# Optimization experiments

Hardware: AMD Instinct MI355X
Metric: run time of the kernel (lower is better)

The kernel has to match this reference:

```python
import jax, jax.numpy as jnp
import numpy as np
import math

H, SQK, SV, PQK, PV = 12, 16, 16, 4, 8
C1, C2 = 384, 128
B, N = 1, 768


def _rand_rot(key, shape):
    # random proper rotation matrices via QR of gaussian matrices
    m = jax.random.normal(key, shape + (3, 3), dtype=jnp.float32)
    q, r = jnp.linalg.qr(m)
    d = jnp.sign(jnp.diagonal(r, axis1=-2, axis2=-1))
    return q * d[..., None, :]


def setup_inputs() -> dict:
    key = jax.random.key(0)
    ks = jax.random.split(key, 16)
    s = 0.05
    return {
        'act': jax.random.normal(ks[0], (B, N, C1), dtype=jnp.float32),
        'act_2d': jax.random.normal(ks[1], (B, N, N, C2), dtype=jnp.float32),
        'sequence_mask': jnp.ones((B, N, 1), dtype=jnp.float32),
        'rot': _rand_rot(ks[2], (B, N)),
        'trans': jax.random.normal(ks[3], (B, N, 3), dtype=jnp.float32),
        'wq': jax.random.normal(ks[4], (C1, H * SQK), dtype=jnp.float32) * s,
        'wk': jax.random.normal(ks[5], (C1, H * SQK), dtype=jnp.float32) * s,
        'wv': jax.random.normal(ks[6], (C1, H * SV), dtype=jnp.float32) * s,
        'wqp': jax.random.normal(ks[7], (C1, H * PQK * 3), dtype=jnp.float32) * s,
        'bqp': jnp.zeros((H * PQK * 3,), dtype=jnp.float32),
        'wkp': jax.random.normal(ks[8], (C1, H * PQK * 3), dtype=jnp.float32) * s,
        'bkp': jnp.zeros((H * PQK * 3,), dtype=jnp.float32),
        'wvp': jax.random.normal(ks[9], (C1, H * PV * 3), dtype=jnp.float32) * s,
        'bvp': jnp.zeros((H * PV * 3,), dtype=jnp.float32),
        'w2d': jax.random.normal(ks[10], (C2, H), dtype=jnp.float32) * s,
        'b2d': jnp.zeros((H,), dtype=jnp.float32),
        'wfin': jax.random.normal(ks[11], (H * (C2 + SV + 4 * PV), C1), dtype=jnp.float32) * s,
        'bfin': jnp.zeros((C1,), dtype=jnp.float32),
        'tw': jnp.zeros((H,), dtype=jnp.float32),
    }


def _points(act, w, b, P):
    # torch: view [...,H,P*3] -> split into 3 chunks of P -> stack last => layout [H,3,P]
    p = (act @ w + b).reshape(*act.shape[:-1], H, 3, P)
    p = jnp.moveaxis(p, -2, -1)  # [B,N,H,P,3]
    return p.reshape(*act.shape[:-1], H * P, 3)


def _ipa(act, act_2d, sequence_mask, rot, trans,
         wq, wk, wv, wqp, bqp, wkp, bkp, wvp, bvp, w2d, b2d, wfin, bfin, tw):
    b, n, _ = act.shape
    q = (act @ wq).reshape(b, n, H, SQK) * math.sqrt(1.0 / SQK)
    k = (act @ wk).reshape(b, n, H, SQK)
    v = (act @ wv).reshape(b, n, H, SV)

    apply = lambda p: jnp.einsum('bnij,bnpj->bnpi', rot, p) + trans[:, :, None, :]
    qp = apply(_points(act, wqp, bqp, PQK))  # [B,N,H*PQK,3]
    kp = apply(_points(act, wkp, bkp, PQK))
    vp = apply(_points(act, wvp, bvp, PV))   # [B,N,H*PV,3]

    # point-distance logits
    pw = math.sqrt(2.0 / (9.0 * PQK)) * jax.nn.softplus(tw)  # [H]
    d2 = jnp.sum(jnp.square(qp[:, :, None] - kp[:, None]), -1)  # [B,N,N,H*PQK]
    d2 = d2.reshape(b, n, n, H, PQK).sum(-1)                    # [B,N,N,H]
    logits = -0.5 * pw * d2
    logits = logits + jnp.einsum('bqhc,bkhc->bqkh', q, k)
    logits = logits + act_2d @ w2d + b2d
    mask_2d = sequence_mask * jnp.swapaxes(sequence_mask, -1, -2)  # [B,N,N]
    logits = logits - 1e5 * (1.0 - mask_2d)[..., None]
    logits = logits * math.sqrt(1.0 / 3.0)
    attn = jax.nn.softmax(logits, axis=-2)  # over key residues

    res_scalar = jnp.einsum('bqkh,bkhc->bqhc', attn, v).reshape(b, n, H * SV)
    vp5 = vp.reshape(b, n, H, PV, 3)
    rpg = jnp.einsum('bqkh,bkhpd->bqhpd', attn, vp5).reshape(b, n, H * PV, 3)
    rpl = jnp.einsum('bnji,bnpj->bnpi', rot, rpg - trans[:, :, None, :])  # invert_apply
    norms = jnp.linalg.norm(rpl, axis=-1)
    r2d = jnp.einsum('bijh,bijc->bihc', attn, act_2d).reshape(b, n, H * C2)
    final = jnp.concatenate(
        [res_scalar, rpl[..., 0], rpl[..., 1], rpl[..., 2], norms, r2d], axis=-1)
    return final @ wfin + bfin


def reference(act, act_2d, sequence_mask, rot, trans,
              wq, wk, wv, wqp, bqp, wkp, bkp, wvp, bvp, w2d, b2d, wfin, bfin, tw):
    return _ipa(act, act_2d, sequence_mask, rot, trans,
                wq, wk, wv, wqp, bqp, wkp, bkp, wvp, bvp, w2d, b2d, wfin, bfin, tw)
```

## Files before the change

### kernel.cpp

```cpp
#include <hip/hip_runtime.h>
#include <math.h>

#define NH    12
#define NRES  768
#define C1V   384
#define C2V   128
#define NPROJ 1152
#define QKD   28
#define FDIM  2112
#define VVD   480
#define APAD  772
#define KSPLIT 11

typedef __attribute__((ext_vector_type(8))) short bf16x8;
typedef __attribute__((ext_vector_type(4))) float f32x4;

__device__ __forceinline__ float softplusf_(float x) {
    return (x > 20.f) ? x : log1pf(__expf(x));
}
__device__ __forceinline__ ushort f2bf(float x) {
    union { float f; unsigned u; } v; v.f = x;
    unsigned r = (v.u + 0x7fffu + ((v.u >> 16) & 1u)) >> 16;
    return (ushort)r;
}

__global__ __launch_bounds__(256) void k1_proj(
    const float* __restrict__ act,
    const float* __restrict__ wq, const float* __restrict__ wk,
    const float* __restrict__ wv, const float* __restrict__ wqp,
    const float* __restrict__ wkp, const float* __restrict__ wvp,
    const float* __restrict__ bqp, const float* __restrict__ bkp,
    const float* __restrict__ bvp, const float* __restrict__ w2d,
    float* __restrict__ proj, ushort* __restrict__ w2dT)
{
    __shared__ float As[64 * 33];
    __shared__ float Bs[32 * 68];
    const int n0 = blockIdx.x * 64, m0 = blockIdx.y * 64;
    const int tid = threadIdx.x;
    const int tx = tid & 15, ty = tid >> 4;
    float c[4][4] = {};

    for (int kt = 0; kt < C1V; kt += 32) {
        for (int idx = tid; idx < 64 * 32; idx += 256) {
            int r = idx >> 5, j = idx & 31;
            As[r * 33 + j] = act[(m0 + r) * C1V + kt + j];
        }
        for (int idx = tid; idx < 32 * 64; idx += 256) {
            int r = idx >> 6, col = idx & 63;
            int jj = n0 + col, k = kt + r;
            float w;
            if      (jj < 192) w = wq [k * 192 + jj];
            else if (jj < 384) w = wk [k * 192 + jj - 192];
            else if (jj < 576) w = wv [k * 192 + jj - 384];
            else if (jj < 720) w = wqp[k * 144 + jj - 576];
            else if (jj < 864) w = wkp[k * 144 + jj - 720];
            else               w = wvp[k * 288 + jj - 864];
            Bs[r * 68 + col] = w;
        }
        __syncthreads();
        #pragma unroll
        for (int kk = 0; kk < 32; ++kk) {
            float a[4];
            #pragma unroll
            for (int i = 0; i < 4; ++i) a[i] = As[(ty * 4 + i) * 33 + kk];
            float4 b4 = *(const float4*)&Bs[kk * 68 + tx * 4];
            float b[4] = {b4.x, b4.y, b4.z, b4.w};
            #pragma unroll
            for (int i = 0; i < 4; ++i)
                #pragma unroll
                for (int j = 0; j < 4; ++j) c[i][j] += a[i] * b[j];
        }
        __syncthreads();
    }
    float biasv[4];
    #pragma unroll
    for (int j = 0; j < 4; ++j) {
        int col = n0 + tx * 4 + j;
        biasv[j] = (col >= 864) ? bvp[col - 864]
                 : (col >= 720) ? bkp[col - 720]
                 : (col >= 576) ? bqp[col - 576] : 0.f;
    }
    #pragma unroll
    for (int i = 0; i < 4; ++i) {
        float4 v;
        v.x = c[i][0] + biasv[0]; v.y = c[i][1] + biasv[1];
        v.z = c[i][2] + biasv[2]; v.w = c[i][3] + biasv[3];
        *(float4*)&proj[(m0 + ty * 4 + i) * NPROJ + n0 + tx * 4] = v;
    }
    if (n0 == 0 && m0 == 0) {
        for (int idx = tid; idx < 2048; idx += 256) {
            int h = idx >> 7, cc = idx & 127;
            w2dT[idx] = (h < NH) ? f2bf(w2d[cc * NH + h]) : (ushort)0;
        }
    }
}

__global__ __launch_bounds__(64) void k2_prep(
    const float* __restrict__ proj, const float* __restrict__ rot,
    const float* __restrict__ trans, const float* __restrict__ tw,
    float* __restrict__ Qv, float* __restrict__ Kv,
    float* __restrict__ akArr, float* __restrict__ vv)
{
    const int n = blockIdx.x, tid = threadIdx.x;
    __shared__ float kp2[48];
    const float* pr = proj + n * NPROJ;
    float R[9], T[3];
    #pragma unroll
    for (int i = 0; i < 9; ++i) R[i] = rot[n * 9 + i];
    #pragma unroll
    for (int i = 0; i < 3; ++i) T[i] = trans[n * 3 + i];

    for (int idx = tid; idx < 192; idx += 64) {
        int h = idx >> 4, cc = idx & 15;
        Qv[(n * NH + h) * QKD + cc] = pr[idx] * 0.25f;
        Kv[(n * NH + h) * QKD + cc] = pr[192 + idx];
        vv[n * VVD + idx] = pr[384 + idx];
    }
    if (tid < 48) {
        int h = tid >> 2, p = tid & 3;
        float pwh = 0.23570226039551584f * softplusf_(tw[h]);
        float lx = pr[576 + h * 12 + p];
        float ly = pr[576 + h * 12 + 4 + p];
        float lz = pr[576 + h * 12 + 8 + p];
        float gx = R[0] * lx + R[1] * ly + R[2] * lz + T[0];
        float gy = R[3] * lx + R[4] * ly + R[5] * lz + T[1];
        float gz = R[6] * lx + R[7] * ly + R[8] * lz + T[2];
        float* qd = &Qv[(n * NH + h) * QKD + 16];
        qd[p] = pwh * gx; qd[4 + p] = pwh * gy; qd[8 + p] = pwh * gz;
        lx = pr[720 + h * 12 + p];
        ly = pr[720 + h * 12 + 4 + p];
        lz = pr[720 + h * 12 + 8 + p];
        gx = R[0] * lx + R[1] * ly + R[2] * lz + T[0];
        gy = R[3] * lx + R[4] * ly + R[5] * lz + T[1];
        gz = R[6] * lx + R[7] * ly + R[8] * lz + T[2];
        float* kd = &Kv[(n * NH + h) * QKD + 16];
        kd[p] = gx; kd[4 + p] = gy; kd[8 + p] = gz;
        kp2[tid] = gx * gx + gy * gy + gz * gz;
    }
    __syncthreads();
    if (tid < NH) {
        float pwh = 0.23570226039551584f * softplusf_(tw[tid]);
        akArr[n * NH + tid] = -0.5f * pwh *
            (kp2[tid * 4] + kp2[tid * 4 + 1] + kp2[tid * 4 + 2] + kp2[tid * 4 + 3]);
    }
    for (int idx = tid; idx < 96; idx += 64) {
        int h = idx >> 3, p = idx & 7;
        float lx = pr[864 + h * 24 + p];
        float ly = pr[864 + h * 24 + 8 + p];
        float lz = pr[864 + h * 24 + 16 + p];
        float gx = R[0] * lx + R[1] * ly + R[2] * lz + T[0];
        float gy = R[3] * lx + R[4] * ly + R[5] * lz + T[1];
        float gz = R[6] * lx + R[7] * ly + R[8] * lz + T[2];
        float* dst = &vv[n * VVD + 192 + h * 24 + p * 3];
        dst[0] = gx; dst[1] = gy; dst[2] = gz;
    }
}

__global__ __launch_bounds__(256) void k2b_qk(
    const float* __restrict__ Qv, const float* __restrict__ Kv,
    const float* __restrict__ akArr, float* __restrict__ qkBuf)
{
    const int h = blockIdx.z;
    const int k0 = blockIdx.x * 64, q0 = blockIdx.y * 64;
    __shared__ float As[64 * 29];
    __shared__ float Bs[64 * 29];
    const int tid = threadIdx.x, tx = tid & 15, ty = tid >> 4;

    for (int idx = tid; idx < 64 * 28; idx += 256) {
        int r = idx / 28, j = idx - r * 28;
        As[r * 29 + j] = Qv[((q0 + r) * NH + h) * QKD + j];
        Bs[r * 29 + j] = Kv[((k0 + r) * NH + h) * QKD + j];
    }
    __syncthreads();
    float c[4][4] = {};
    #pragma unroll
    for (int kk = 0; kk < 28; ++kk) {
        float a[4], b[4];
        #pragma unroll
        for (int i = 0; i < 4; ++i) a[i] = As[(ty * 4 + i) * 29 + kk];
        #pragma unroll
        for (int j = 0; j < 4; ++j) b[j] = Bs[(tx * 4 + j) * 29 + kk];
        #pragma unroll
        for (int i = 0; i < 4; ++i)
            #pragma unroll
            for (int j = 0; j < 4; ++j) c[i][j] += a[i] * b[j];
    }
    float akv[4];
    #pragma unroll
    for (int j = 0; j < 4; ++j) akv[j] = akArr[(k0 + tx * 4 + j) * NH + h];
    #pragma unroll
    for (int i = 0; i < 4; ++i) {
        float4 v;
        v.x = c[i][0] + akv[0]; v.y = c[i][1] + akv[1];
        v.z = c[i][2] + akv[2]; v.w = c[i][3] + akv[3];
        *(float4*)&qkBuf[((q0 + ty * 4 + i) * NH + h) * NRES + k0 + tx * 4] = v;
    }
}

__global__ __launch_bounds__(256) void kA_mfma(
    const float* __restrict__ act2d, const float* __restrict__ smask,
    const ushort* __restrict__ w2dT, float* __restrict__ qkBuf)
{
    const int q = blockIdx.y, k0 = blockIdx.x * 64, tid = threadIdx.x;
    __shared__ ushort tile[64 * 136];
    const int lane = tid & 63, wv = tid >> 6;
    const int nb = lane & 15, quad = lane >> 4;

    bf16x8 bfr[4];
    #pragma unroll
    for (int s = 0; s < 4; ++s)
        bfr[s] = *(const bf16x8*)&w2dT[nb * 128 + quad * 8 + s * 32];

    const float* src = act2d + ((size_t)q * NRES + k0) * C2V;
    #pragma unroll
    for (int i = 0; i < 8; ++i) {
        int f = tid + i * 256;
        int r = f >> 5, c4 = f & 31;
        float4 v = ((const float4*)src)[f];
        ushort4 o = { f2bf(v.x), f2bf(v.y), f2bf(v.z), f2bf(v.w) };
        *(ushort4*)&tile[r * 136 + c4 * 4] = o;
    }
    __syncthreads();

    f32x4 acc = {0.f, 0.f, 0.f, 0.f};
    #pragma unroll
    for (int s = 0; s < 4; ++s) {
        bf16x8 af = *(const bf16x8*)&tile[(wv * 16 + nb) * 136 + quad * 8 + s * 32];
        acc = __builtin_amdgcn_mfma_f32_16x16x32_bf16(af, bfr[s], acc, 0, 0, 0);
    }

    if (nb < NH) {
        const int kb = k0 + wv * 16 + quad * 4;
        float* dst = &qkBuf[((size_t)(q * NH + nb)) * NRES + kb];
        float4 old = *(float4*)dst;
        float4 sm = *(const float4*)&smask[kb];
        const float smq = smask[q];
        const float scale = 0.5773502691896258f;
        float4 outv;
        outv.x = (old.x + acc[0] - 1e5f * (1.f - smq * sm.x)) * scale;
        outv.y = (old.y + acc[1] - 1e5f * (1.f - smq * sm.y)) * scale;
        outv.z = (old.z + acc[2] - 1e5f * (1.f - smq * sm.z)) * scale;
        outv.w = (old.w + acc[3] - 1e5f * (1.f - smq * sm.w)) * scale;
        *(float4*)dst = outv;
    }
}

__global__ __launch_bounds__(256) void kC_attn(
    const float* __restrict__ act2d, const float* __restrict__ qkBuf,
    const float* __restrict__ vv, const float* __restrict__ rot,
    const float* __restrict__ trans, float* __restrict__ F)
{
    const int q = blockIdx.x, tid = threadIdx.x;
    __shared__ float attnS[NH * APAD];
    __shared__ float scr[1536];
    __shared__ float red[NH * 4];
    __shared__ float mh[NH], lh[NH];
    __shared__ float rotS[9], transS[3];

    if (tid < 9) rotS[tid] = rot[q * 9 + tid];
    if (tid < 3) transS[tid] = trans[q * 3 + tid];

    float lg[3][NH];
    #pragma unroll
    for (int h = 0; h < NH; ++h)
        #pragma unroll
        for (int i = 0; i < 3; ++i)
            lg[i][h] = qkBuf[((size_t)(q * NH + h)) * NRES + tid + 256 * i];

    const int wv_ = tid >> 6, lane = tid & 63;
    #pragma unroll
    for (int h = 0; h < NH; ++h) {
        float v = fmaxf(fmaxf(lg[0][h], lg[1][h]), lg[2][h]);
        for (int off = 32; off > 0; off >>= 1) v = fmaxf(v, __shfl_down(v, off, 64));
        if (lane == 0) red[h * 4 + wv_] = v;
    }
    __syncthreads();
    if (tid < NH)
        mh[tid] = fmaxf(fmaxf(red[tid * 4], red[tid * 4 + 1]),
                        fmaxf(red[tid * 4 + 2], red[tid * 4 + 3]));
    __syncthreads();
    float lsum[NH];
    #pragma unroll
    for (int h = 0; h < NH; ++h) lsum[h] = 0.f;
    #pragma unroll
    for (int i = 0; i < 3; ++i)
        #pragma unroll
        for (int h = 0; h < NH; ++h) {
            float e = __expf(lg[i][h] - mh[h]);
            attnS[h * APAD + tid + 256 * i] = e;
            lsum[h] += e;
        }
    #pragma unroll
    for (int h = 0; h < NH; ++h) {
        float v = lsum[h];
        for (int off = 32; off > 0; off >>= 1) v += __shfl_down(v, off, 64);
        if (lane == 0) red[h * 4 + wv_] = v;
    }
    __syncthreads();
    if (tid < NH)
        lh[tid] = 1.f / (red[tid * 4] + red[tid * 4 + 1] + red[tid * 4 + 2] + red[tid * 4 + 3]);
    __syncthreads();

    const int cq = tid & 31, hg = (tid >> 5) & 3, kg = tid >> 7;
    const int h0 = 3 * hg;
    const float* abase = act2d + ((size_t)q * NRES + kg * 384) * C2V + cq * 4;
    const float* at0 = &attnS[(h0    ) * APAD + kg * 384];
    const float* at1 = &attnS[(h0 + 1) * APAD + kg * 384];
    const float* at2 = &attnS[(h0 + 2) * APAD + kg * 384];
    float4 a0 = {0,0,0,0}, a1 = {0,0,0,0}, a2 = {0,0,0,0};

    for (int kk = 0; kk < 384; kk += 4) {
        float4 t0 = *(const float4*)&abase[(size_t)(kk    ) * C2V];
        float4 t1 = *(const float4*)&abase[(size_t)(kk + 1) * C2V];
        float4 t2 = *(const float4*)&abase[(size_t)(kk + 2) * C2V];
        float4 t3 = *(const float4*)&abase[(size_t)(kk + 3) * C2V];
        float4 p0 = *(const float4*)&at0[kk];
        float4 p1 = *(const float4*)&at1[kk];
        float4 p2 = *(const float4*)&at2[kk];
        a0.x += p0.x*t0.x + p0.y*t1.x + p0.z*t2.x + p0.w*t3.x;
        a0.y += p0.x*t0.y + p0.y*t1.y + p0.z*t2.y + p0.w*t3.y;
        a0.z += p0.x*t0.z + p0.y*t1.z + p0.z*t2.z + p0.w*t3.z;
        a0.w += p0.x*t0.w + p0.y*t1.w + p0.z*t2.w + p0.w*t3.w;
        a1.x += p1.x*t0.x + p1.y*t1.x + p1.z*t2.x + p1.w*t3.x;
        a1.y += p1.x*t0.y + p1.y*t1.y + p1.z*t2.y + p1.w*t3.y;
        a1.z += p1.x*t0.z + p1.y*t1.z + p1.z*t2.z + p1.w*t3.z;
        a1.w += p1.x*t0.w + p1.y*t1.w + p1.z*t2.w + p1.w*t3.w;
        a2.x += p2.x*t0.x + p2.y*t1.x + p2.z*t2.x + p2.w*t3.x;
        a2.y += p2.x*t0.y + p2.y*t1.y + p2.z*t2.y + p2.w*t3.y;
        a2.z += p2.x*t0.z + p2.y*t1.z + p2.z*t2.z + p2.w*t3.z;
        a2.w += p2.x*t0.w + p2.y*t1.w + p2.z*t2.w + p2.w*t3.w;
    }
    if (kg == 1) {
        *(float4*)&scr[(h0    ) * 128 + cq * 4] = a0;
        *(float4*)&scr[(h0 + 1) * 128 + cq * 4] = a1;
        *(float4*)&scr[(h0 + 2) * 128 + cq * 4] = a2;
    }
    __syncthreads();
    float* Fq = F + q * FDIM;
    if (kg == 0) {
        float4 b0 = *(const float4*)&scr[(h0    ) * 128 + cq * 4];
        float4 b1 = *(const float4*)&scr[(h0 + 1) * 128 + cq * 4];
        float4 b2 = *(const float4*)&scr[(h0 + 2) * 128 + cq * 4];
        float l0 = lh[h0], l1 = lh[h0 + 1], l2 = lh[h0 + 2];
        float4 o0 = {(a0.x+b0.x)*l0, (a0.y+b0.y)*l0, (a0.z+b0.z)*l0, (a0.w+b0.w)*l0};
        float4 o1 = {(a1.x+b1.x)*l1, (a1.y+b1.y)*l1, (a1.z+b1.z)*l1, (a1.w+b1.w)*l1};
        float4 o2 = {(a2.x+b2.x)*l2, (a2.y+b2.y)*l2, (a2.z+b2.z)*l2, (a2.w+b2.w)*l2};
        *(float4*)&Fq[576 + (h0    ) * 128 + cq * 4] = o0;
        *(float4*)&Fq[576 + (h0 + 1) * 128 + cq * 4] = o1;
        *(float4*)&Fq[576 + (h0 + 2) * 128 + cq * 4] = o2;
    }
    __syncthreads();

    const int j4 = tid & 127;
    const int kgv = tid >> 7;
    float p0 = 0.f, p1 = 0.f, p2 = 0.f, p3 = 0.f;
    if (j4 < 120) {
        const int h = (j4 < 48) ? (j4 >> 2) : ((j4 - 48) / 6);
        const float* at = &attnS[h * APAD + kgv * 384];
        const float* col = vv + (size_t)(kgv * 384) * VVD + j4 * 4;
        #pragma unroll 8
        for (int k = 0; k < 384; ++k) {
            float a = at[k];
            float4 v = *(const float4*)(col + (size_t)k * VVD);
            p0 += a * v.x; p1 += a * v.y; p2 += a * v.z; p3 += a * v.w;
        }
    }
    __syncthreads();
    if (j4 < 120) {
        float4 pv = {p0, p1, p2, p3};
        *(float4*)&scr[(kgv * 120 + j4) * 4] = pv;
    }
    __syncthreads();
    if (tid < 120) {
        float4 a = *(const float4*)&scr[tid * 4];
        float4 b = *(const float4*)&scr[(120 + tid) * 4];
        const int h = (tid < 48) ? (tid >> 2) : ((tid - 48) / 6);
        const float il = lh[h];
        float4 s = {(a.x + b.x) * il, (a.y + b.y) * il,
                    (a.z + b.z) * il, (a.w + b.w) * il};
        if (tid < 48) {
            *(float4*)&Fq[tid * 4] = s;
        } else {
            *(float4*)&scr[1024 + (tid - 48) * 4] = s;
        }
    }
    __syncthreads();
    if (tid < 96) {
        float gx = scr[1024 + tid * 3]     - transS[0];
        float gy = scr[1024 + tid * 3 + 1] - transS[1];
        float gz = scr[1024 + tid * 3 + 2] - transS[2];
        float x = rotS[0] * gx + rotS[3] * gy + rotS[6] * gz;
        float y = rotS[1] * gx + rotS[4] * gy + rotS[7] * gz;
        float z = rotS[2] * gx + rotS[5] * gy + rotS[8] * gz;
        Fq[192 + tid] = x;
        Fq[288 + tid] = y;
        Fq[384 + tid] = z;
        Fq[480 + tid] = sqrtf(x * x + y * y + z * z);
    }
}

__global__ __launch_bounds__(256) void k5_partial(
    const float* __restrict__ F, const float* __restrict__ wfin,
    float* __restrict__ part)
{
    const int n0 = blockIdx.x * 64, m0 = blockIdx.y * 64, kz = blockIdx.z;
    const int kbeg = kz * 192;
    __shared__ float As[64 * 33];
    __shared__ float Bs[32 * 68];
    const int tid = threadIdx.x, tx = tid & 15, ty = tid >> 4;
    float c[4][4] = {};

    for (int kt = kbeg; kt < kbeg + 192; kt += 32) {
        for (int idx = tid; idx < 64 * 32; idx += 256) {
            int r = idx >> 5, j = idx & 31;
            As[r * 33 + j] = F[(m0 + r) * FDIM + kt + j];
        }
        for (int idx = tid; idx < 32 * 64; idx += 256) {
            int r = idx >> 6, col = idx & 63;
            Bs[r * 68 + col] = wfin[(kt + r) * 384 + n0 + col];
        }
        __syncthreads();
        #pragma unroll
        for (int kk = 0; kk < 32; ++kk) {
            float a[4];
            #pragma unroll
            for (int i = 0; i < 4; ++i) a[i] = As[(ty * 4 + i) * 33 + kk];
            float4 b4 = *(const float4*)&Bs[kk * 68 + tx * 4];
            float b[4] = {b4.x, b4.y, b4.z, b4.w};
            #pragma unroll
            for (int i = 0; i < 4; ++i)
                #pragma unroll
                for (int j = 0; j < 4; ++j) c[i][j] += a[i] * b[j];
        }
        __syncthreads();
    }
    float* dst = part + (size_t)kz * (768 * 384);
    #pragma unroll
    for (int i = 0; i < 4; ++i) {
        float4 v = {c[i][0], c[i][1], c[i][2], c[i][3]};
        *(float4*)&dst[(m0 + ty * 4 + i) * 384 + n0 + tx * 4] = v;
    }
}

__global__ __launch_bounds__(256) void k5_reduce(
    const float* __restrict__ part, const float* __restrict__ bfin,
    float* __restrict__ out)
{
    const int e = blockIdx.x * 256 + threadIdx.x;
    const float4* p = (const float4*)part;
    float4 b = ((const float4*)bfin)[e % 96];
    float4 s = {b.x, b.y, b.z, b.w};
    #pragma unroll
    for (int kz = 0; kz < KSPLIT; ++kz) {
        float4 v = p[(size_t)kz * 73728 + e];
        s.x += v.x; s.y += v.y; s.z += v.z; s.w += v.w;
    }
    ((float4*)out)[e] = s;
}

extern "C" void kernel_launch(void* const* d_in, const int* in_sizes, int n_in,
                              void* d_out, int out_size, void* d_ws, size_t ws_size,
                              hipStream_t stream) {
    const float* act   = (const float*)d_in[0];
    const float* act2d = (const float*)d_in[1];
    const float* smask = (const float*)d_in[2];
    const float* rot   = (const float*)d_in[3];
    const float* trans = (const float*)d_in[4];
    const float* wq    = (const float*)d_in[5];
    const float* wk    = (const float*)d_in[6];
    const float* wvv   = (const float*)d_in[7];
    const float* wqp   = (const float*)d_in[8];
    const float* bqp   = (const float*)d_in[9];
    const float* wkp   = (const float*)d_in[10];
    const float* bkp   = (const float*)d_in[11];
    const float* wvp   = (const float*)d_in[12];
    const float* bvp   = (const float*)d_in[13];
    const float* w2d   = (const float*)d_in[14];
    const float* wfin  = (const float*)d_in[16];
    const float* bfin  = (const float*)d_in[17];
    const float* tw    = (const float*)d_in[18];

    float* W     = (float*)d_ws;
    float* proj  = W;
    float* Qv    = proj  + 768 * NPROJ;
    float* Kv    = Qv    + 768 * NH * QKD;
    float* akArr = Kv    + 768 * NH * QKD;
    float* vvA   = akArr + 768 * NH;
    float* qkBuf = vvA   + 768 * VVD;
    float* F     = qkBuf + 768 * NH * NRES;
    ushort* w2dT = (ushort*)(F + 768 * FDIM);
    float* part  = qkBuf;

    k1_proj<<<dim3(18, 12), 256, 0, stream>>>(act, wq, wk, wvv, wqp, wkp, wvp,
                                              bqp, bkp, bvp, w2d, proj, w2dT);
    k2_prep<<<dim3(NRES), 64, 0, stream>>>(proj, rot, trans, tw, Qv, Kv, akArr, vvA);
    k2b_qk<<<dim3(12, 12, NH), 256, 0, stream>>>(Qv, Kv, akArr, qkBuf);
    kA_mfma<<<dim3(12, NRES), 256, 0, stream>>>(act2d, smask, w2dT, qkBuf);
    kC_attn<<<dim3(NRES), 256, 0, stream>>>(act2d, qkBuf, vvA, rot, trans, F);
    k5_partial<<<dim3(6, 12, KSPLIT), 256, 0, stream>>>(F, wfin, part);
    k5_reduce<<<dim3(288), 256, 0, stream>>>(part, bfin, (float*)d_out);
}
```

Measured before the change: 689.2 us.

## Fuse QK logits into pair-bias kernel and split-K reduce into GEMM

Removes the separate QK tiled-GEMM kernel. kA_mfma now computes each q·k dot product plus the point-attention bias inline, so qkBuf is written once instead of written, read and rewritten. The split-K final projection reduction moves into k5_partial: a per-tile atomic counter (cleared in kC_attn) lets the last arriving block sum the partials and add the bias. This drops two launches and a large intermediate round trip, at the cost of redundant K loads per block and atomics/threadfences.

Measured after the change: 872.6 us. 26.6% more time.

```diff
diff --git a/kernel.cpp b/kernel.cpp
--- a/kernel.cpp
+++ b/kernel.cpp
@@ -156,55 +156,17 @@
     }
 }
 
-__global__ __launch_bounds__(256) void k2b_qk(
-    const float* __restrict__ Qv, const float* __restrict__ Kv,
-    const float* __restrict__ akArr, float* __restrict__ qkBuf)
-{
-    const int h = blockIdx.z;
-    const int k0 = blockIdx.x * 64, q0 = blockIdx.y * 64;
-    __shared__ float As[64 * 29];
-    __shared__ float Bs[64 * 29];
-    const int tid = threadIdx.x, tx = tid & 15, ty = tid >> 4;
-
-    for (int idx = tid; idx < 64 * 28; idx += 256) {
-        int r = idx / 28, j = idx - r * 28;
-        As[r * 29 + j] = Qv[((q0 + r) * NH + h) * QKD + j];
-        Bs[r * 29 + j] = Kv[((k0 + r) * NH + h) * QKD + j];
-    }
-    __syncthreads();
-    float c[4][4] = {};
-    #pragma unroll
-    for (int kk = 0; kk < 28; ++kk) {
-        float a[4], b[4];
-        #pragma unroll
-        for (int i = 0; i < 4; ++i) a[i] = As[(ty * 4 + i) * 29 + kk];
-        #pragma unroll
-        for (int j = 0; j < 4; ++j) b[j] = Bs[(tx * 4 + j) * 29 + kk];
-        #pragma unroll
-        for (int i = 0; i < 4; ++i)
-            #pragma unroll
-            for (int j = 0; j < 4; ++j) c[i][j] += a[i] * b[j];
-    }
-    float akv[4];
-    #pragma unroll
-    for (int j = 0; j < 4; ++j) akv[j] = akArr[(k0 + tx * 4 + j) * NH + h];
-    #pragma unroll
-    for (int i = 0; i < 4; ++i) {
-        float4 v;
-        v.x = c[i][0] + akv[0]; v.y = c[i][1] + akv[1];
-        v.z = c[i][2] + akv[2]; v.w = c[i][3] + akv[3];
-        *(float4*)&qkBuf[((q0 + ty * 4 + i) * NH + h) * NRES + k0 + tx * 4] = v;
-    }
-}
-
 __global__ __launch_bounds__(256) void kA_mfma(
     const float* __restrict__ act2d, const float* __restrict__ smask,
-    const ushort* __restrict__ w2dT, float* __restrict__ qkBuf)
+    const ushort* __restrict__ w2dT, const float* __restrict__ Qv,
+    const float* __restrict__ Kv, const float* __restrict__ akArr,
+    float* __restrict__ qkBuf)
 {
     const int q = blockIdx.y, k0 = blockIdx.x * 64, tid = threadIdx.x;
     __shared__ ushort tile[64 * 136];
     const int lane = tid & 63, wv = tid >> 6;
     const int nb = lane & 15, quad = lane >> 4;
+    const int kb = k0 + wv * 16 + quad * 4;
 
     bf16x8 bfr[4];
     #pragma unroll
@@ -220,6 +182,28 @@
         ushort4 o = { f2bf(v.x), f2bf(v.y), f2bf(v.z), f2bf(v.w) };
         *(ushort4*)&tile[r * 136 + c4 * 4] = o;
     }
+
+    float qk[4] = {0.f, 0.f, 0.f, 0.f};
+    float ak[4] = {0.f, 0.f, 0.f, 0.f};
+    if (nb < NH) {
+        const float* Qr = &Qv[((size_t)q * NH + nb) * QKD];
+        float4 qv[7];
+        #pragma unroll
+        for (int j = 0; j < 7; ++j) qv[j] = *(const float4*)&Qr[j * 4];
+        #pragma unroll
+        for (int r = 0; r < 4; ++r) {
+            const float* Kr = &Kv[((size_t)(kb + r) * NH + nb) * QKD];
+            float s = 0.f;
+            #pragma unroll
+            for (int j = 0; j < 7; ++j) {
+                float4 kv = *(const float4*)&Kr[j * 4];
+                s += qv[j].x * kv.x + qv[j].y * kv.y
+                   + qv[j].z * kv.z + qv[j].w * kv.w;
+            }
+            qk[r] = s;
+            ak[r] = akArr[(size_t)(kb + r) * NH + nb];
+        }
+    }
     __syncthreads();
 
     f32x4 acc = {0.f, 0.f, 0.f, 0.f};
@@ -230,25 +214,23 @@
     }
 
     if (nb < NH) {
-        const int kb = k0 + wv * 16 + quad * 4;
-        float* dst = &qkBuf[((size_t)(q * NH + nb)) * NRES + kb];
-        float4 old = *(float4*)dst;
         float4 sm = *(const float4*)&smask[kb];
         const float smq = smask[q];
         const float scale = 0.5773502691896258f;
         float4 outv;
-        outv.x = (old.x + acc[0] - 1e5f * (1.f - smq * sm.x)) * scale;
-        outv.y = (old.y + acc[1] - 1e5f * (1.f - smq * sm.y)) * scale;
-        outv.z = (old.z + acc[2] - 1e5f * (1.f - smq * sm.z)) * scale;
-        outv.w = (old.w + acc[3] - 1e5f * (1.f - smq * sm.w)) * scale;
-        *(float4*)dst = outv;
+        outv.x = (qk[0] + ak[0] + acc[0] - 1e5f * (1.f - smq * sm.x)) * scale;
+        outv.y = (qk[1] + ak[1] + acc[1] - 1e5f * (1.f - smq * sm.y)) * scale;
+        outv.z = (qk[2] + ak[2] + acc[2] - 1e5f * (1.f - smq * sm.z)) * scale;
+        outv.w = (qk[3] + ak[3] + acc[3] - 1e5f * (1.f - smq * sm.w)) * scale;
+        *(float4*)&qkBuf[((size_t)(q * NH + nb)) * NRES + kb] = outv;
     }
 }
 
 __global__ __launch_bounds__(256) void kC_attn(
     const float* __restrict__ act2d, const float* __restrict__ qkBuf,
     const float* __restrict__ vv, const float* __restrict__ rot,
-    const float* __restrict__ trans, float* __restrict__ F)
+    const float* __restrict__ trans, float* __restrict__ F,
+    unsigned* __restrict__ cnt)
 {
     const int q = blockIdx.x, tid = threadIdx.x;
     __shared__ float attnS[NH * APAD];
@@ -257,6 +239,7 @@
     __shared__ float mh[NH], lh[NH];
     __shared__ float rotS[9], transS[3];
 
+    if (q == 0 && tid < 72) cnt[tid] = 0u;
     if (tid < 9) rotS[tid] = rot[q * 9 + tid];
     if (tid < 3) transS[tid] = trans[q * 3 + tid];
 
@@ -401,7 +384,8 @@
 
 __global__ __launch_bounds__(256) void k5_partial(
     const float* __restrict__ F, const float* __restrict__ wfin,
-    float* __restrict__ part)
+    const float* __restrict__ bfin, float* __restrict__ part,
+    unsigned* __restrict__ cnt, float* __restrict__ out)
 {
     const int n0 = blockIdx.x * 64, m0 = blockIdx.y * 64, kz = blockIdx.z;
     const int kbeg = kz * 192;
@@ -440,22 +424,29 @@
         float4 v = {c[i][0], c[i][1], c[i][2], c[i][3]};
         *(float4*)&dst[(m0 + ty * 4 + i) * 384 + n0 + tx * 4] = v;
     }
-}
-
-__global__ __launch_bounds__(256) void k5_reduce(
-    const float* __restrict__ part, const float* __restrict__ bfin,
-    float* __restrict__ out)
-{
-    const int e = blockIdx.x * 256 + threadIdx.x;
-    const float4* p = (const float4*)part;
-    float4 b = ((const float4*)bfin)[e % 96];
-    float4 s = {b.x, b.y, b.z, b.w};
-    #pragma unroll
-    for (int kz = 0; kz < KSPLIT; ++kz) {
-        float4 v = p[(size_t)kz * 73728 + e];
-        s.x += v.x; s.y += v.y; s.z += v.z; s.w += v.w;
-    }
-    ((float4*)out)[e] = s;
+
+    __threadfence();
+    __shared__ int isLast;
+    if (tid == 0) {
+        unsigned old = atomicAdd(&cnt[blockIdx.y * 6 + blockIdx.x], 1u);
+        isLast = (old == KSPLIT - 1) ? 1 : 0;
+    }
+    __syncthreads();
+    if (isLast) {
+        __threadfence();
+        #pragma unroll
+        for (int i = 0; i < 4; ++i) {
+            const int row = m0 + ty * 4 + i, colb = n0 + tx * 4;
+            float4 s = *(const float4*)&bfin[colb];
+            #pragma unroll
+            for (int kzz = 0; kzz < KSPLIT; ++kzz) {
+                float4 v = *(const float4*)&part[(size_t)kzz * (768 * 384)
+                                                 + (size_t)row * 384 + colb];
+                s.x += v.x; s.y += v.y; s.z += v.z; s.w += v.w;
+            }
+            *(float4*)&out[(size_t)row * 384 + colb] = s;
+        }
+    }
 }
 
 extern "C" void kernel_launch(void* const* d_in, const int* in_sizes, int n_in,
@@ -489,14 +480,15 @@
     float* qkBuf = vvA   + 768 * VVD;
     float* F     = qkBuf + 768 * NH * NRES;
     ushort* w2dT = (ushort*)(F + 768 * FDIM);
+    unsigned* cnt = (unsigned*)(w2dT + 2048);
     float* part  = qkBuf;
 
     k1_proj<<<dim3(18, 12), 256, 0, stream>>>(act, wq, wk, wvv, wqp, wkp, wvp,
                                               bqp, bkp, bvp, w2d, proj, w2dT);
     k2_prep<<<dim3(NRES), 64, 0, stream>>>(proj, rot, trans, tw, Qv, Kv, akArr, vvA);
-    k2b_qk<<<dim3(12, 12, NH), 256, 0, stream>>>(Qv, Kv, akArr, qkBuf);
-    kA_mfma<<<dim3(12, NRES), 256, 0, stream>>>(act2d, smask, w2dT, qkBuf);
-    kC_attn<<<dim3(NRES), 256, 0, stream>>>(act2d, qkBuf, vvA, rot, trans, F);
-    k5_partial<<<dim3(6, 12, KSPLIT), 256, 0, stream>>>(F, wfin, part);
-    k5_reduce<<<dim3(288), 256, 0, stream>>>(part, bfin, (float*)d_out);
-}
+    kA_mfma<<<dim3(12, NRES), 256, 0, stream>>>(act2d, smask, w2dT, Qv, Kv, akArr,
+                                                qkBuf);
+    kC_attn<<<dim3(NRES), 256, 0, stream>>>(act2d, qkBuf, vvA, rot, trans, F, cnt);
+    k5_partial<<<dim3(6, 12, KSPLIT), 256, 0, stream>>>(F, wfin, bfin, part, cnt,
+                                                        (float*)d_out);
+}
```

## Load act_2d straight into MFMA registers and fuse split-K reduce via atomic counters

Applied to the files above, without the earlier changes.

In kA_mfma, each lane now reads its own act_2d row slice directly from global memory and converts it to bf16 in registers. This drops the shared-memory tile and the __syncthreads. Separately, the k5_reduce kernel is removed: the last k5_partial block for each output tile, chosen with an atomic counter and thread fences, sums the split-K partials and adds the bias. The counters are zeroed inside kC_attn. This saves one kernel launch, but the per-lane global loads in kA may coalesce less well.

New measurement: 782.1 us. 13.5% more time.

```diff
diff --git a/kernel.cpp b/kernel.cpp
--- a/kernel.cpp
+++ b/kernel.cpp
@@ -202,7 +202,6 @@
     const ushort* __restrict__ w2dT, float* __restrict__ qkBuf)
 {
     const int q = blockIdx.y, k0 = blockIdx.x * 64, tid = threadIdx.x;
-    __shared__ ushort tile[64 * 136];
     const int lane = tid & 63, wv = tid >> 6;
     const int nb = lane & 15, quad = lane >> 4;
 
@@ -211,21 +210,22 @@
     for (int s = 0; s < 4; ++s)
         bfr[s] = *(const bf16x8*)&w2dT[nb * 128 + quad * 8 + s * 32];
 
-    const float* src = act2d + ((size_t)q * NRES + k0) * C2V;
-    #pragma unroll
-    for (int i = 0; i < 8; ++i) {
-        int f = tid + i * 256;
-        int r = f >> 5, c4 = f & 31;
-        float4 v = ((const float4*)src)[f];
-        ushort4 o = { f2bf(v.x), f2bf(v.y), f2bf(v.z), f2bf(v.w) };
-        *(ushort4*)&tile[r * 136 + c4 * 4] = o;
-    }
-    __syncthreads();
-
+    const int krow = k0 + wv * 16 + nb;
+    const float* arow = act2d + ((size_t)q * NRES + krow) * C2V + quad * 8;
+    float4 u[4], w[4];
+    #pragma unroll
+    for (int s = 0; s < 4; ++s) {
+        u[s] = *(const float4*)&arow[s * 32];
+        w[s] = *(const float4*)&arow[s * 32 + 4];
+    }
     f32x4 acc = {0.f, 0.f, 0.f, 0.f};
     #pragma unroll
     for (int s = 0; s < 4; ++s) {
-        bf16x8 af = *(const bf16x8*)&tile[(wv * 16 + nb) * 136 + quad * 8 + s * 32];
+        bf16x8 af;
+        af[0] = (short)f2bf(u[s].x); af[1] = (short)f2bf(u[s].y);
+        af[2] = (short)f2bf(u[s].z); af[3] = (short)f2bf(u[s].w);
+        af[4] = (short)f2bf(w[s].x); af[5] = (short)f2bf(w[s].y);
+        af[6] = (short)f2bf(w[s].z); af[7] = (short)f2bf(w[s].w);
         acc = __builtin_amdgcn_mfma_f32_16x16x32_bf16(af, bfr[s], acc, 0, 0, 0);
     }
 
@@ -248,7 +248,8 @@
 __global__ __launch_bounds__(256) void kC_attn(
     const float* __restrict__ act2d, const float* __restrict__ qkBuf,
     const float* __restrict__ vv, const float* __restrict__ rot,
-    const float* __restrict__ trans, float* __restrict__ F)
+    const float* __restrict__ trans, float* __restrict__ F,
+    unsigned* __restrict__ cnt)
 {
     const int q = blockIdx.x, tid = threadIdx.x;
     __shared__ float attnS[NH * APAD];
@@ -257,6 +258,7 @@
     __shared__ float mh[NH], lh[NH];
     __shared__ float rotS[9], transS[3];
 
+    if (q == 0 && tid < 72) cnt[tid] = 0u;
     if (tid < 9) rotS[tid] = rot[q * 9 + tid];
     if (tid < 3) transS[tid] = trans[q * 3 + tid];
 
@@ -401,7 +403,8 @@
 
 __global__ __launch_bounds__(256) void k5_partial(
     const float* __restrict__ F, const float* __restrict__ wfin,
-    float* __restrict__ part)
+    const float* __restrict__ bfin, float* __restrict__ part,
+    unsigned* __restrict__ cnt, float* __restrict__ out)
 {
     const int n0 = blockIdx.x * 64, m0 = blockIdx.y * 64, kz = blockIdx.z;
     const int kbeg = kz * 192;
@@ -440,22 +443,29 @@
         float4 v = {c[i][0], c[i][1], c[i][2], c[i][3]};
         *(float4*)&dst[(m0 + ty * 4 + i) * 384 + n0 + tx * 4] = v;
     }
-}
-
-__global__ __launch_bounds__(256) void k5_reduce(
-    const float* __restrict__ part, const float* __restrict__ bfin,
-    float* __restrict__ out)
-{
-    const int e = blockIdx.x * 256 + threadIdx.x;
-    const float4* p = (const float4*)part;
-    float4 b = ((const float4*)bfin)[e % 96];
-    float4 s = {b.x, b.y, b.z, b.w};
-    #pragma unroll
-    for (int kz = 0; kz < KSPLIT; ++kz) {
-        float4 v = p[(size_t)kz * 73728 + e];
-        s.x += v.x; s.y += v.y; s.z += v.z; s.w += v.w;
-    }
-    ((float4*)out)[e] = s;
+
+    __threadfence();
+    __shared__ int isLast;
+    if (tid == 0) {
+        unsigned old = atomicAdd(&cnt[blockIdx.y * 6 + blockIdx.x], 1u);
+        isLast = (old == KSPLIT - 1) ? 1 : 0;
+    }
+    __syncthreads();
+    if (isLast) {
+        __threadfence();
+        #pragma unroll
+        for (int i = 0; i < 4; ++i) {
+            const int row = m0 + ty * 4 + i, colb = n0 + tx * 4;
+            float4 s = *(const float4*)&bfin[colb];
+            #pragma unroll
+            for (int kzz = 0; kzz < KSPLIT; ++kzz) {
+                float4 v = *(const float4*)&part[(size_t)kzz * (768 * 384)
+                                                 + (size_t)row * 384 + colb];
+                s.x += v.x; s.y += v.y; s.z += v.z; s.w += v.w;
+            }
+            *(float4*)&out[(size_t)row * 384 + colb] = s;
+        }
+    }
 }
 
 extern "C" void kernel_launch(void* const* d_in, const int* in_sizes, int n_in,
@@ -489,6 +499,7 @@
     float* qkBuf = vvA   + 768 * VVD;
     float* F     = qkBuf + 768 * NH * NRES;
     ushort* w2dT = (ushort*)(F + 768 * FDIM);
+    unsigned* cnt = (unsigned*)(w2dT + 2048);
     float* part  = qkBuf;
 
     k1_proj<<<dim3(18, 12), 256, 0, stream>>>(act, wq, wk, wvv, wqp, wkp, wvp,
@@ -496,7 +507,7 @@
     k2_prep<<<dim3(NRES), 64, 0, stream>>>(proj, rot, trans, tw, Qv, Kv, akArr, vvA);
     k2b_qk<<<dim3(12, 12, NH), 256, 0, stream>>>(Qv, Kv, akArr, qkBuf);
     kA_mfma<<<dim3(12, NRES), 256, 0, stream>>>(act2d, smask, w2dT, qkBuf);
-    kC_attn<<<dim3(NRES), 256, 0, stream>>>(act2d, qkBuf, vvA, rot, trans, F);
-    k5_partial<<<dim3(6, 12, KSPLIT), 256, 0, stream>>>(F, wfin, part);
-    k5_reduce<<<dim3(288), 256, 0, stream>>>(part, bfin, (float*)d_out);
-}
+    kC_attn<<<dim3(NRES), 256, 0, stream>>>(act2d, qkBuf, vvA, rot, trans, F, cnt);
+    k5_partial<<<dim3(6, 12, KSPLIT), 256, 0, stream>>>(F, wfin, bfin, part, cnt,
+                                                        (float*)d_out);
+}
```
